# Kernel optimization log

Hardware: AMD Instinct MI355X
Metric: run time of the kernel (lower is better)

The kernel has to match this reference:

```python
import jax, jax.numpy as jnp
import numpy as np

V, BLK, L, H, C, FF = 50257, 2048, 6, 8, 512, 2048
D = C // H  # head_dim = 64

def setup_inputs() -> dict:
    key = jax.random.key(0)
    ks = jax.random.split(key, 16)
    s = 0.02
    proj_std = 0.02 / np.sqrt(2 * L)
    return {
        'idx': jax.random.randint(ks[0], (2, 2048), 0, V, dtype=jnp.int64),
        'wte': jax.random.normal(ks[1], (V, C), jnp.float32) * s,
        'wpe': jax.random.normal(ks[2], (BLK, C), jnp.float32) * s,
        'ln1_w': jnp.ones((L, C), jnp.float32), 'ln1_b': jnp.zeros((L, C), jnp.float32),
        'c_attn_w': jax.random.normal(ks[3], (L, 3 * C, C), jnp.float32) * s,
        'c_proj_w': jax.random.normal(ks[4], (L, C, C), jnp.float32) * proj_std,
        'ln2_w': jnp.ones((L, C), jnp.float32), 'ln2_b': jnp.zeros((L, C), jnp.float32),
        'fc_w': jax.random.normal(ks[5], (L, FF, C), jnp.float32) * s,
        'proj_w': jax.random.normal(ks[6], (L, C, FF), jnp.float32) * proj_std,
        'lnf_w': jnp.ones((C,), jnp.float32), 'lnf_b': jnp.zeros((C,), jnp.float32),
    }

def _layernorm(x, w, b, eps=1e-5):
    mu = jnp.mean(x, axis=-1, keepdims=True)
    var = jnp.var(x, axis=-1, keepdims=True)
    return (x - mu) * jax.lax.rsqrt(var + eps) * w + b

def _attn(x, attn_w, proj_w, mask):
    B, T, _ = x.shape
    qkv = jnp.einsum('btc,fc->btf', x, attn_w)  # (B,T,3C)
    q, k, v = jnp.split(qkv, 3, axis=-1)
    q = q.reshape(B, T, H, D)
    k = k.reshape(B, T, H, D)
    v = v.reshape(B, T, H, D)
    scale = 1.0 / np.sqrt(D)
    att = jnp.einsum('bthd,bshd->bhts', q, k) * scale  # (B,H,T,T)
    att = jnp.where(mask, att, -jnp.inf)
    att = jax.nn.softmax(att, axis=-1)
    y = jnp.einsum('bhts,bshd->bthd', att, v).reshape(B, T, C)
    return jnp.einsum('btc,oc->bto', y, proj_w)

def reference(idx, wte, wpe, ln1_w, ln1_b, c_attn_w, c_proj_w, ln2_w, ln2_b, fc_w, proj_w, lnf_w, lnf_b):
    B, T = idx.shape
    pos = jnp.arange(T)
    x = wte[idx] + wpe[pos]  # (B,T,C); dropout p=0
    mask = jnp.tril(jnp.ones((T, T), bool))[None, None]
    for i in range(L):
        x = x + _attn(_layernorm(x, ln1_w[i], ln1_b[i]), c_attn_w[i], c_proj_w[i], mask)
        h = _layernorm(x, ln2_w[i], ln2_b[i])
        h = jax.nn.gelu(jnp.einsum('btc,fc->btf', h, fc_w[i]), approximate=False)
        x = x + jnp.einsum('btf,cf->btc', h, proj_w[i])
    x = _layernorm(x, lnf_w, lnf_b)
    logits = jnp.einsum('btc,vc->btv', x, wte)  # tied lm_head
    return logits
```

## Files before the change

### kernel.cpp

```cpp
#include <hip/hip_runtime.h>

typedef unsigned short u16;
typedef short bf16x8 __attribute__((ext_vector_type(8)));
typedef float f32x4 __attribute__((ext_vector_type(4)));
typedef unsigned short u16x4 __attribute__((ext_vector_type(4)));
typedef unsigned short u16x8 __attribute__((ext_vector_type(8)));
typedef unsigned int u32x2 __attribute__((ext_vector_type(2)));

#define B_ 2
#define T_ 2048
#define C_ 512
#define H_ 8
#define FF_ 2048
#define L_ 6
#define V_ 50257
#define M_ (B_*T_)

__device__ __forceinline__ u16 f2b(float f) {
  union { float f; unsigned u; } v; v.f = f;
  unsigned r = v.u + 0x7FFFu + ((v.u >> 16) & 1u);
  return (u16)(r >> 16);
}
__device__ __forceinline__ float b2f(u16 u) {
  union { unsigned u; float f; } v; v.u = ((unsigned)u) << 16; return v.f;
}
__device__ __forceinline__ unsigned pk_bf16(float lo, float hi) {
  unsigned r;
  asm volatile("v_cvt_pk_bf16_f32 %0, %1, %2" : "=v"(r) : "v"(lo), "v"(hi));
  return r;
}

__device__ __forceinline__ void async16(const void* g, void* l) {
  __builtin_amdgcn_global_load_lds((const __attribute__((address_space(1))) unsigned int*)g,
                                   (__attribute__((address_space(3))) unsigned int*)l, 16, 0, 0);
}

template<int N> __device__ __forceinline__ void vwait() {
  if constexpr (N == 0) asm volatile("s_waitcnt vmcnt(0)" ::: "memory");
  else if constexpr (N == 2) asm volatile("s_waitcnt vmcnt(2)" ::: "memory");
  else if constexpr (N == 3) asm volatile("s_waitcnt vmcnt(3)" ::: "memory");
  else if constexpr (N == 4) asm volatile("s_waitcnt vmcnt(4)" ::: "memory");
}

__device__ __forceinline__ bf16x8 scale8(u16x8 v, float s) {
  union { bf16x8 b; unsigned u[4]; } r;
#pragma unroll
  for (int i = 0; i < 4; i++)
    r.u[i] = pk_bf16(b2f(v[2*i]) * s, b2f(v[2*i+1]) * s);
  return r.b;
}

struct CvtArgs { const f32x4* s[5]; u16x4* d[5]; };
__global__ void cvt_all_k(CvtArgs a) {
  const int sizes[5] = { V_*C_/4, L_*3*C_*C_/4, L_*C_*C_/4, L_*FF_*C_/4, L_*C_*FF_/4 };
  int gid = blockIdx.x * blockDim.x + threadIdx.x;
  int stride = gridDim.x * blockDim.x;
#pragma unroll
  for (int seg = 0; seg < 5; seg++) {
    const f32x4* src = a.s[seg];
    u16x4* dst = a.d[seg];
    for (int i = gid; i < sizes[seg]; i += stride) {
      f32x4 v = src[i];
      u16x4 o;
      o[0] = f2b(v[0]); o[1] = f2b(v[1]); o[2] = f2b(v[2]); o[3] = f2b(v[3]);
      dst[i] = o;
    }
  }
}

__global__ void embed_k(const int* __restrict__ idx, const float* __restrict__ wte,
                        const float* __restrict__ wpe, float* __restrict__ x) {
  int t = blockIdx.x * 256 + threadIdx.x;
  int row = t >> 7;
  int c4 = t & 127;
  int tok = idx[row];
  int pos = row & (T_ - 1);
  f32x4 a = ((const f32x4*)(wte + (long)tok * C_))[c4];
  f32x4 p = ((const f32x4*)(wpe + (long)pos * C_))[c4];
  ((f32x4*)x)[t] = a + p;
}

__global__ void ln_k(const float* __restrict__ x, const float* __restrict__ w,
                     const float* __restrict__ b, u16* __restrict__ out) {
  int wv = threadIdx.x >> 6;
  int lane = threadIdx.x & 63;
  int row = blockIdx.x * 4 + wv;
  const f32x4* xr = (const f32x4*)(x + (long)row * C_);
  f32x4 v0 = xr[lane * 2], v1 = xr[lane * 2 + 1];
  float s = 0.f, s2 = 0.f;
#pragma unroll
  for (int j = 0; j < 4; j++) { s += v0[j] + v1[j]; s2 += v0[j]*v0[j] + v1[j]*v1[j]; }
#pragma unroll
  for (int off = 32; off >= 1; off >>= 1) { s += __shfl_xor(s, off); s2 += __shfl_xor(s2, off); }
  float mu = s * (1.f / C_);
  float inv = rsqrtf(s2 * (1.f / C_) - mu * mu + 1e-5f);
  const f32x4* wr = (const f32x4*)w;
  const f32x4* br = (const f32x4*)b;
  f32x4 w0 = wr[lane*2], w1 = wr[lane*2+1], b0 = br[lane*2], b1 = br[lane*2+1];
  u16x8 o;
#pragma unroll
  for (int j = 0; j < 4; j++) {
    o[j]     = f2b((v0[j] - mu) * inv * w0[j] + b0[j]);
    o[j + 4] = f2b((v1[j] - mu) * inv * w1[j] + b1[j]);
  }
  *(u16x8*)(out + (long)row * C_ + lane * 8) = o;
}

template<int EPI, int BM, int BN>
__global__ __launch_bounds__(256) void gemm_bt_k(
    const u16* __restrict__ A, const u16* __restrict__ Bw,
    u16* __restrict__ Cb, float* __restrict__ Cf,
    int N, int K, int ldc)
{
  constexpr int MT = BM / 32;
  constexpr int NT = BN / 32;
  constexpr int AJ = BM / 64;
  constexpr int BJ = BN / 64;
  constexpr int LPT = AJ + BJ;
  __shared__ __align__(16) u16 sA[3][BM * 32];
  __shared__ __align__(16) u16 sB[3][BN * 32];
  const int tid = threadIdx.x;
  const int n0 = blockIdx.x * BN;
  const int m0 = blockIdx.y * BM;
  const int w = tid >> 6;
  const int lane = tid & 63;
  const int wm = (w >> 1) * (BM / 2);
  const int wn = (w & 1) * (BN / 2);
  const int g = lane >> 4;
  const int l15 = lane & 15;
  const int sw3 = l15 & 3;

  f32x4 acc[MT][NT] = {};

  const int nk = K >> 5;
  const int ksw = ((tid & 3) ^ ((tid >> 2) & 3)) * 8;
  const u16* gA[AJ];
  const u16* gB[BJ];
#pragma unroll
  for (int j = 0; j < AJ; j++)
    gA[j] = A + (long)(m0 + (tid >> 2) + j * 64) * K + ksw;
#pragma unroll
  for (int j = 0; j < BJ; j++)
    gB[j] = Bw + (long)(n0 + (tid >> 2) + j * 64) * K + ksw;

  auto stage = [&](int buf, int kt) {
    int ko = kt << 5;
#pragma unroll
    for (int j = 0; j < AJ; j++)
      async16(gA[j] + ko, &sA[buf][(j * 256 + w * 64) * 8]);
#pragma unroll
    for (int j = 0; j < BJ; j++)
      async16(gB[j] + ko, &sB[buf][(j * 256 + w * 64) * 8]);
  };

  stage(0, 0);
  stage(1, 1);
  int cur = 0, nxt = 2;
  for (int kt = 0; kt < nk; kt++) {
    if (kt + 1 < nk) vwait<LPT>(); else vwait<0>();
    __builtin_amdgcn_s_barrier();
    if (kt + 2 < nk) stage(nxt, kt + 2);
    const u16* pa = sA[cur];
    const u16* pb = sB[cur];
    bf16x8 af[MT], bfr[NT];
#pragma unroll
    for (int mt = 0; mt < MT; mt++)
      af[mt] = *(const bf16x8*)(pa + (wm + mt * 16 + l15) * 32 + ((g ^ sw3) * 8));
#pragma unroll
    for (int nt = 0; nt < NT; nt++)
      bfr[nt] = *(const bf16x8*)(pb + (wn + nt * 16 + l15) * 32 + ((g ^ sw3) * 8));
#pragma unroll
    for (int mt = 0; mt < MT; mt++)
#pragma unroll
      for (int nt = 0; nt < NT; nt++)
        acc[mt][nt] = __builtin_amdgcn_mfma_f32_16x16x32_bf16(af[mt], bfr[nt], acc[mt][nt], 0, 0, 0);
    cur = (cur == 2) ? 0 : cur + 1;
    nxt = (nxt == 2) ? 0 : nxt + 1;
  }

#pragma unroll
  for (int mt = 0; mt < MT; mt++) {
    int m = m0 + wm + mt * 16 + g * 4;
#pragma unroll
    for (int nt = 0; nt < NT; nt++) {
      int n = n0 + wn + nt * 16 + l15;
      f32x4 v = acc[mt][nt];
#pragma unroll
      for (int r = 0; r < 4; r++) {
        long ci = (long)(m + r) * ldc + n;
        if (EPI == 0) {
          Cb[ci] = f2b(v[r]);
        } else if (EPI == 1) {
          Cf[ci] += v[r];
        } else {
          float f = v[r];
          f = 0.5f * f * (1.0f + erff(f * 0.70710678118654752f));
          Cb[ci] = f2b(f);
        }
      }
    }
  }
}

__global__ __launch_bounds__(512) void gemm_lmhead_k(
    const u16* __restrict__ A, const u16* __restrict__ Bw,
    float* __restrict__ Cf, int N)
{
  __shared__ __align__(16) u16 sA[3][256 * 32];
  __shared__ __align__(16) u16 sB[3][128 * 32];
  const int K = 512;
  const int bid = blockIdx.x;
  const int swz = (bid & 7) * 786 + (bid >> 3);
  const int n0 = (swz % 393) * 128;
  const int m0 = (swz / 393) * 256;
  const int tid = threadIdx.x;
  const int w = tid >> 6;
  const int lane = tid & 63;
  const int wm = (w >> 1) * 64;
  const int wn = (w & 1) * 64;
  const int g = lane >> 4;
  const int l15 = lane & 15;
  const int sw3 = l15 & 3;

  f32x4 acc[4][4] = {};

  const int ksw = ((tid & 3) ^ ((tid >> 2) & 3)) * 8;
  const u16* gA[2];
#pragma unroll
  for (int j = 0; j < 2; j++)
    gA[j] = A + (long)(m0 + (tid >> 2) + j * 128) * K + ksw;
  int brow = n0 + (tid >> 2); if (brow > N - 1) brow = N - 1;
  const u16* gB0 = Bw + (long)brow * K + ksw;

  auto stage = [&](int buf, int kt) {
    int ko = kt << 5;
#pragma unroll
    for (int j = 0; j < 2; j++)
      async16(gA[j] + ko, &sA[buf][(j * 512 + w * 64) * 8]);
    async16(gB0 + ko, &sB[buf][(w * 64) * 8]);
  };

  stage(0, 0);
  stage(1, 1);
  int cur = 0, nxt = 2;
  const int nk = K >> 5;
  for (int kt = 0; kt < nk; kt++) {
    if (kt + 1 < nk) vwait<3>(); else vwait<0>();
    __builtin_amdgcn_s_barrier();
    if (kt + 2 < nk) stage(nxt, kt + 2);
    const u16* pa = sA[cur];
    const u16* pb = sB[cur];
    bf16x8 af[4], bfr[4];
#pragma unroll
    for (int mt = 0; mt < 4; mt++)
      af[mt] = *(const bf16x8*)(pa + (wm + mt * 16 + l15) * 32 + ((g ^ sw3) * 8));
#pragma unroll
    for (int nt = 0; nt < 4; nt++)
      bfr[nt] = *(const bf16x8*)(pb + (wn + nt * 16 + l15) * 32 + ((g ^ sw3) * 8));
#pragma unroll
    for (int mt = 0; mt < 4; mt++)
#pragma unroll
      for (int nt = 0; nt < 4; nt++)
        acc[mt][nt] = __builtin_amdgcn_mfma_f32_16x16x32_bf16(af[mt], bfr[nt], acc[mt][nt], 0, 0, 0);
    cur = (cur == 2) ? 0 : cur + 1;
    nxt = (nxt == 2) ? 0 : nxt + 1;
  }

#pragma unroll
  for (int mt = 0; mt < 4; mt++) {
    int m = m0 + wm + mt * 16 + g * 4;
#pragma unroll
    for (int nt = 0; nt < 4; nt++) {
      int n = n0 + wn + nt * 16 + l15;
      f32x4 v = acc[mt][nt];
      if (n < N) {
#pragma unroll
        for (int r = 0; r < 4; r++)
          Cf[(long)(m + r) * N + n] = v[r];
      }
    }
  }
}

__global__ __launch_bounds__(128) void attn_k(const u16* __restrict__ qkv, u16* __restrict__ out) {
  const int bh = blockIdx.y;
  const int b = bh >> 3;
  const int h = bh & 7;
  const int tid = threadIdx.x;
  const int wv = tid >> 6;
  const int lane = tid & 63;
  const int g = lane >> 4;
  const int l15 = lane & 15;
  const int qblk = 31 - (blockIdx.x >> 1);
  const int halfsel = blockIdx.x & 1;

  __shared__ __align__(16) u16 Ks[2][64 * 64];
  __shared__ __align__(16) u16 Vt[2][64 * 72];
  __shared__ __align__(16) u16 Ps[2][16 * 64];

  const long base = (long)b * T_ * 1536;
  const u16* kbase = qkv + base + 512 + h * 64;
  const u16* vbase = qkv + base + 1024 + h * 64;
  const int kq = tid & 15;
  const int dg = tid >> 4;
  const float qscale = 0.18033688011112042f;

  const int q0 = qblk * 64 + halfsel * 32 + wv * 16;

  const u16* qrow = qkv + base + (long)(q0 + l15) * 1536 + h * 64;
  bf16x8 qf0 = scale8(*(const u16x8*)(qrow + g * 8), qscale);
  bf16x8 qf1 = scale8(*(const u16x8*)(qrow + 32 + g * 8), qscale);

  f32x4 o[4] = {};
  float mrun[4] = {-1e30f, -1e30f, -1e30f, -1e30f};
  float lrun[4] = {0.f, 0.f, 0.f, 0.f};
  const int kvend = qblk * 64 + 64;

  u16x8 vreg[4];
#pragma unroll
  for (int i = 0; i < 4; i++) {
    int chunk = i * 128 + tid;
    int row = chunk >> 3, c8 = chunk & 7;
    async16(kbase + (long)row * 1536 + (c8 ^ (row & 7)) * 8,
            &Ks[0][(i * 128 + wv * 64) * 8]);
  }
#pragma unroll
  for (int t = 0; t < 4; t++)
    vreg[t] = *(const u16x8*)(vbase + (long)(kq + 16 * t) * 1536 + dg * 8);
#pragma unroll
  for (int e = 0; e < 8; e++) {
    int d = dg * 8 + e;
    u32x2 wq = { (unsigned)vreg[0][e] | ((unsigned)vreg[1][e] << 16),
                 (unsigned)vreg[2][e] | ((unsigned)vreg[3][e] << 16) };
    *(u32x2*)(&Vt[0][d * 72 + kq * 4]) = wq;
  }
  __syncthreads();

  int cur = 0;
  for (int j0 = 0; j0 < kvend; j0 += 64, cur ^= 1) {
    const bool more = (j0 + 64) < kvend;
    if (more) {
      int jn = j0 + 64;
#pragma unroll
      for (int i = 0; i < 4; i++) {
        int chunk = i * 128 + tid;
        int row = chunk >> 3, c8 = chunk & 7;
        async16(kbase + (long)(jn + row) * 1536 + (c8 ^ (row & 7)) * 8,
                &Ks[cur ^ 1][(i * 128 + wv * 64) * 8]);
      }
#pragma unroll
      for (int t = 0; t < 4; t++)
        vreg[t] = *(const u16x8*)(vbase + (long)(jn + kq + 16 * t) * 1536 + dg * 8);
    }

    f32x4 s[4] = {};
    const u16* kp = Ks[cur];
#pragma unroll
    for (int t = 0; t < 4; t++) {
      int row = t * 16 + l15;
      const u16* kr = kp + row * 64;
      bf16x8 k0 = *(const bf16x8*)(kr + ((g ^ (row & 7)) * 8));
      bf16x8 k1 = *(const bf16x8*)(kr + (((4 + g) ^ (row & 7)) * 8));
      s[t] = __builtin_amdgcn_mfma_f32_16x16x32_bf16(qf0, k0, s[t], 0, 0, 0);
      s[t] = __builtin_amdgcn_mfma_f32_16x16x32_bf16(qf1, k1, s[t], 0, 0, 0);
    }

    const bool diag = (j0 + 64) == kvend;
    u16* pw = Ps[wv];
#pragma unroll
    for (int r = 0; r < 4; r++) {
      int row = q0 + g * 4 + r;
      float v0 = s[0][r], v1 = s[1][r], v2 = s[2][r], v3 = s[3][r];
      if (diag) {
        if (j0 +      l15 > row) v0 = -1e30f;
        if (j0 + 16 + l15 > row) v1 = -1e30f;
        if (j0 + 32 + l15 > row) v2 = -1e30f;
        if (j0 + 48 + l15 > row) v3 = -1e30f;
      }
      float mloc = fmaxf(fmaxf(v0, v1), fmaxf(v2, v3));
      float m = mrun[r];
      if (!__all(mloc <= m + 8.0f)) {
        float mx = mloc;
        mx = fmaxf(mx, __shfl_xor(mx, 1));
        mx = fmaxf(mx, __shfl_xor(mx, 2));
        mx = fmaxf(mx, __shfl_xor(mx, 4));
        mx = fmaxf(mx, __shfl_xor(mx, 8));
        float mn = fmaxf(m, mx);
        float sc2 = exp2f(m - mn);
        lrun[r] *= sc2;
#pragma unroll
        for (int dt = 0; dt < 4; dt++) o[dt][r] *= sc2;
        m = mn; mrun[r] = mn;
      }
      float e0 = exp2f(v0 - m), e1 = exp2f(v1 - m);
      float e2 = exp2f(v2 - m), e3 = exp2f(v3 - m);
      lrun[r] += (e0 + e1) + (e2 + e3);
      u32x2 pkq = { pk_bf16(e0, e1), pk_bf16(e2, e3) };
      int prow = g * 4 + r;
      int byt = prow * 128 + ((((l15 >> 1) ^ (prow & 7)) << 4)) + (l15 & 1) * 8;
      *(u32x2*)((char*)pw + byt) = pkq;
    }

    const u16* vt = Vt[cur];
    bf16x8 pf0 = *(const bf16x8*)((char*)pw + l15 * 128 + (((g) ^ (l15 & 7)) << 4));
    bf16x8 pf1 = *(const bf16x8*)((char*)pw + l15 * 128 + (((4 + g) ^ (l15 & 7)) << 4));
#pragma unroll
    for (int dt = 0; dt < 4; dt++) {
      int d = dt * 16 + l15;
      bf16x8 vf0 = *(const bf16x8*)(vt + d * 72 + g * 8);
      bf16x8 vf1 = *(const bf16x8*)(vt + d * 72 + 32 + g * 8);
      o[dt] = __builtin_amdgcn_mfma_f32_16x16x32_bf16(pf0, vf0, o[dt], 0, 0, 0);
      o[dt] = __builtin_amdgcn_mfma_f32_16x16x32_bf16(pf1, vf1, o[dt], 0, 0, 0);
    }

    if (more) {
#pragma unroll
      for (int e = 0; e < 8; e++) {
        int d = dg * 8 + e;
        u32x2 wq = { (unsigned)vreg[0][e] | ((unsigned)vreg[1][e] << 16),
                     (unsigned)vreg[2][e] | ((unsigned)vreg[3][e] << 16) };
        *(u32x2*)(&Vt[cur ^ 1][d * 72 + kq * 4]) = wq;
      }
    }
    __syncthreads();
  }

#pragma unroll
  for (int r = 0; r < 4; r++) {
    float ls = lrun[r];
    ls += __shfl_xor(ls, 1); ls += __shfl_xor(ls, 2);
    ls += __shfl_xor(ls, 4); ls += __shfl_xor(ls, 8);
    float inv = 1.0f / ls;
    int row = q0 + g * 4 + r;
    u16* orow = out + (long)(b * T_ + row) * C_ + h * 64;
#pragma unroll
    for (int dt = 0; dt < 4; dt++)
      orow[dt * 16 + l15] = f2b(o[dt][r] * inv);
  }
}

extern "C" void kernel_launch(void* const* d_in, const int* in_sizes, int n_in,
                              void* d_out, int out_size, void* d_ws, size_t ws_size,
                              hipStream_t stream) {
  const int*   idx    = (const int*)  d_in[0];
  const float* wte    = (const float*)d_in[1];
  const float* wpe    = (const float*)d_in[2];
  const float* ln1w   = (const float*)d_in[3];
  const float* ln1b   = (const float*)d_in[4];
  const float* wattn  = (const float*)d_in[5];
  const float* wcproj = (const float*)d_in[6];
  const float* ln2w   = (const float*)d_in[7];
  const float* ln2b   = (const float*)d_in[8];
  const float* wfc    = (const float*)d_in[9];
  const float* wproj2 = (const float*)d_in[10];
  const float* lnfw   = (const float*)d_in[11];
  const float* lnfb   = (const float*)d_in[12];
  float* out = (float*)d_out;

  char* p = (char*)d_ws;
  size_t off = 0;
  auto alloc = [&](size_t bytes) -> void* {
    void* r = p + off; off += (bytes + 255) & ~(size_t)255; return r;
  };
  float* x    = (float*)alloc((size_t)M_ * C_ * 4);
  u16* xn     = (u16*)alloc((size_t)M_ * C_ * 2);
  u16* qkvb   = (u16*)alloc((size_t)M_ * 3 * C_ * 2);
  u16* attb   = (u16*)alloc((size_t)M_ * C_ * 2);
  u16* hb     = (u16*)alloc((size_t)M_ * FF_ * 2);
  u16* wteB   = (u16*)alloc((size_t)V_ * C_ * 2);
  u16* wattnB = (u16*)alloc((size_t)L_ * 3 * C_ * C_ * 2);
  u16* wprojB = (u16*)alloc((size_t)L_ * C_ * C_ * 2);
  u16* wfcB   = (u16*)alloc((size_t)L_ * FF_ * C_ * 2);
  u16* wp2B   = (u16*)alloc((size_t)L_ * C_ * FF_ * 2);
  if (off > ws_size) return;

  CvtArgs ca;
  ca.s[0] = (const f32x4*)wte;    ca.d[0] = (u16x4*)wteB;
  ca.s[1] = (const f32x4*)wattn;  ca.d[1] = (u16x4*)wattnB;
  ca.s[2] = (const f32x4*)wcproj; ca.d[2] = (u16x4*)wprojB;
  ca.s[3] = (const f32x4*)wfc;    ca.d[3] = (u16x4*)wfcB;
  ca.s[4] = (const f32x4*)wproj2; ca.d[4] = (u16x4*)wp2B;
  cvt_all_k<<<dim3(2048), dim3(256), 0, stream>>>(ca);

  embed_k<<<dim3(M_ * C_ / 4 / 256), dim3(256), 0, stream>>>(idx, wte, wpe, x);

  for (int l = 0; l < L_; l++) {
    ln_k<<<dim3(M_ / 4), dim3(256), 0, stream>>>(x, ln1w + l * C_, ln1b + l * C_, xn);
    gemm_bt_k<0, 64, 128><<<dim3(12, 64), dim3(256), 0, stream>>>(
        xn, wattnB + (size_t)l * 3 * C_ * C_, qkvb, nullptr, 3 * C_, C_, 3 * C_);
    attn_k<<<dim3(64, B_ * H_), dim3(128), 0, stream>>>(qkvb, attb);
    gemm_bt_k<1, 64, 64><<<dim3(8, 64), dim3(256), 0, stream>>>(
        attb, wprojB + (size_t)l * C_ * C_, nullptr, x, C_, C_, C_);
    ln_k<<<dim3(M_ / 4), dim3(256), 0, stream>>>(x, ln2w + l * C_, ln2b + l * C_, xn);
    gemm_bt_k<2, 128, 128><<<dim3(16, 32), dim3(256), 0, stream>>>(
        xn, wfcB + (size_t)l * FF_ * C_, hb, nullptr, FF_, C_, FF_);
    gemm_bt_k<1, 64, 64><<<dim3(8, 64), dim3(256), 0, stream>>>(
        hb, wp2B + (size_t)l * C_ * FF_, nullptr, x, C_, FF_, C_);
  }
  ln_k<<<dim3(M_ / 4), dim3(256), 0, stream>>>(x, lnfw, lnfb, xn);
  gemm_lmhead_k<<<dim3(8 * 786), dim3(512), 0, stream>>>(xn, wteB, out, V_);
}
```

Measured before the change: 1.380 ms.

## Share K/V tiles across 4 waves in attention and use fast exp/tanh-GELU

Attention blocks now process 64 query rows with 256 threads instead of 32 rows with 128, so each K/V tile loaded into LDS serves twice as many queries and redundant global traffic drops. Softmax exponentials use the hardware v_exp_f32 instead of exp2f. The FC GELU epilogue replaces erff with a tanh-form approximation built from a fast exp and reciprocal, which slightly changes numerics relative to the exact erf GELU. The larger blocks halve the attention grid, which may reduce occupancy or load balance.

```diff
diff --git a/kernel.cpp b/kernel.cpp
--- a/kernel.cpp
+++ b/kernel.cpp
@@ -28,6 +28,12 @@
   unsigned r;
   asm volatile("v_cvt_pk_bf16_f32 %0, %1, %2" : "=v"(r) : "v"(lo), "v"(hi));
   return r;
+}
+__device__ __forceinline__ float exp2_fast(float x) {
+  float r; asm("v_exp_f32 %0, %1" : "=v"(r) : "v"(x)); return r;
+}
+__device__ __forceinline__ float rcp_fast(float x) {
+  float r; asm("v_rcp_f32 %0, %1" : "=v"(r) : "v"(x)); return r;
 }
 
 __device__ __forceinline__ void async16(const void* g, void* l) {
@@ -194,8 +200,11 @@
           Cf[ci] += v[r];
         } else {
           float f = v[r];
-          f = 0.5f * f * (1.0f + erff(f * 0.70710678118654752f));
-          Cb[ci] = f2b(f);
+          float u = f * f;
+          float inner = f * (0.7978845608028654f + 0.03567740814183056f * u);
+          inner = fminf(fmaxf(inner, -15.f), 15.f);
+          float a = exp2_fast(2.8853900817779268f * inner);
+          Cb[ci] = f2b(f * a * rcp_fast(a + 1.0f));
         }
       }
     }
@@ -282,7 +291,7 @@
   }
 }
 
-__global__ __launch_bounds__(128) void attn_k(const u16* __restrict__ qkv, u16* __restrict__ out) {
+__global__ __launch_bounds__(256) void attn_k(const u16* __restrict__ qkv, u16* __restrict__ out) {
   const int bh = blockIdx.y;
   const int b = bh >> 3;
   const int h = bh & 7;
@@ -291,21 +300,20 @@
   const int lane = tid & 63;
   const int g = lane >> 4;
   const int l15 = lane & 15;
-  const int qblk = 31 - (blockIdx.x >> 1);
-  const int halfsel = blockIdx.x & 1;
+  const int qblk = 31 - blockIdx.x;
 
   __shared__ __align__(16) u16 Ks[2][64 * 64];
   __shared__ __align__(16) u16 Vt[2][64 * 72];
-  __shared__ __align__(16) u16 Ps[2][16 * 64];
+  __shared__ __align__(16) u16 Ps[4][16 * 64];
 
   const long base = (long)b * T_ * 1536;
   const u16* kbase = qkv + base + 512 + h * 64;
   const u16* vbase = qkv + base + 1024 + h * 64;
   const int kq = tid & 15;
-  const int dg = tid >> 4;
+  const int dg = (tid >> 4) & 7;
   const float qscale = 0.18033688011112042f;
 
-  const int q0 = qblk * 64 + halfsel * 32 + wv * 16;
+  const int q0 = qblk * 64 + wv * 16;
 
   const u16* qrow = qkv + base + (long)(q0 + l15) * 1536 + h * 64;
   bf16x8 qf0 = scale8(*(const u16x8*)(qrow + g * 8), qscale);
@@ -318,21 +326,23 @@
 
   u16x8 vreg[4];
 #pragma unroll
-  for (int i = 0; i < 4; i++) {
-    int chunk = i * 128 + tid;
+  for (int i = 0; i < 2; i++) {
+    int chunk = i * 256 + tid;
     int row = chunk >> 3, c8 = chunk & 7;
     async16(kbase + (long)row * 1536 + (c8 ^ (row & 7)) * 8,
-            &Ks[0][(i * 128 + wv * 64) * 8]);
-  }
-#pragma unroll
-  for (int t = 0; t < 4; t++)
-    vreg[t] = *(const u16x8*)(vbase + (long)(kq + 16 * t) * 1536 + dg * 8);
-#pragma unroll
-  for (int e = 0; e < 8; e++) {
-    int d = dg * 8 + e;
-    u32x2 wq = { (unsigned)vreg[0][e] | ((unsigned)vreg[1][e] << 16),
-                 (unsigned)vreg[2][e] | ((unsigned)vreg[3][e] << 16) };
-    *(u32x2*)(&Vt[0][d * 72 + kq * 4]) = wq;
+            &Ks[0][(i * 256 + wv * 64) * 8]);
+  }
+  if (tid < 128) {
+#pragma unroll
+    for (int t = 0; t < 4; t++)
+      vreg[t] = *(const u16x8*)(vbase + (long)(kq + 16 * t) * 1536 + dg * 8);
+#pragma unroll
+    for (int e = 0; e < 8; e++) {
+      int d = dg * 8 + e;
+      u32x2 wq = { (unsigned)vreg[0][e] | ((unsigned)vreg[1][e] << 16),
+                   (unsigned)vreg[2][e] | ((unsigned)vreg[3][e] << 16) };
+      *(u32x2*)(&Vt[0][d * 72 + kq * 4]) = wq;
+    }
   }
   __syncthreads();
 
@@ -342,15 +352,17 @@
     if (more) {
       int jn = j0 + 64;
 #pragma unroll
-      for (int i = 0; i < 4; i++) {
-        int chunk = i * 128 + tid;
+      for (int i = 0; i < 2; i++) {
+        int chunk = i * 256 + tid;
         int row = chunk >> 3, c8 = chunk & 7;
         async16(kbase + (long)(jn + row) * 1536 + (c8 ^ (row & 7)) * 8,
-                &Ks[cur ^ 1][(i * 128 + wv * 64) * 8]);
-      }
-#pragma unroll
-      for (int t = 0; t < 4; t++)
-        vreg[t] = *(const u16x8*)(vbase + (long)(jn + kq + 16 * t) * 1536 + dg * 8);
+                &Ks[cur ^ 1][(i * 256 + wv * 64) * 8]);
+      }
+      if (tid < 128) {
+#pragma unroll
+        for (int t = 0; t < 4; t++)
+          vreg[t] = *(const u16x8*)(vbase + (long)(jn + kq + 16 * t) * 1536 + dg * 8);
+      }
     }
 
     f32x4 s[4] = {};
@@ -386,14 +398,14 @@
         mx = fmaxf(mx, __shfl_xor(mx, 4));
         mx = fmaxf(mx, __shfl_xor(mx, 8));
         float mn = fmaxf(m, mx);
-        float sc2 = exp2f(m - mn);
+        float sc2 = exp2_fast(m - mn);
         lrun[r] *= sc2;
 #pragma unroll
         for (int dt = 0; dt < 4; dt++) o[dt][r] *= sc2;
         m = mn; mrun[r] = mn;
       }
-      float e0 = exp2f(v0 - m), e1 = exp2f(v1 - m);
-      float e2 = exp2f(v2 - m), e3 = exp2f(v3 - m);
+      float e0 = exp2_fast(v0 - m), e1 = exp2_fast(v1 - m);
+      float e2 = exp2_fast(v2 - m), e3 = exp2_fast(v3 - m);
       lrun[r] += (e0 + e1) + (e2 + e3);
       u32x2 pkq = { pk_bf16(e0, e1), pk_bf16(e2, e3) };
       int prow = g * 4 + r;
@@ -413,7 +425,7 @@
       o[dt] = __builtin_amdgcn_mfma_f32_16x16x32_bf16(pf1, vf1, o[dt], 0, 0, 0);
     }
 
-    if (more) {
+    if (more && tid < 128) {
 #pragma unroll
       for (int e = 0; e < 8; e++) {
         int d = dg * 8 + e;
@@ -488,7 +500,7 @@
     ln_k<<<dim3(M_ / 4), dim3(256), 0, stream>>>(x, ln1w + l * C_, ln1b + l * C_, xn);
     gemm_bt_k<0, 64, 128><<<dim3(12, 64), dim3(256), 0, stream>>>(
         xn, wattnB + (size_t)l * 3 * C_ * C_, qkvb, nullptr, 3 * C_, C_, 3 * C_);
-    attn_k<<<dim3(64, B_ * H_), dim3(128), 0, stream>>>(qkvb, attb);
+    attn_k<<<dim3(32, B_ * H_), dim3(256), 0, stream>>>(qkvb, attb);
     gemm_bt_k<1, 64, 64><<<dim3(8, 64), dim3(256), 0, stream>>>(
         attb, wprojB + (size_t)l * C_ * C_, nullptr, x, C_, C_, C_);
     ln_k<<<dim3(M_ / 4), dim3(256), 0, stream>>>(x, ln2w + l * C_, ln2b + l * C_, xn);
```

Result: faster. 1.297 ms (-6.0%).
